# Kernel tuning notes

Measured on AMD Instinct MI355X. Metric: run time of the kernel, lower is better.

The kernel has to match this reference:

```python
import jax, jax.numpy as jnp
import numpy as np

TEMPERATURE = 8.0  # sqrt(head_dim=64)

def setup_inputs() -> dict:
    key = jax.random.key(0)
    kq, kk, kv, km = jax.random.split(key, 4)
    B, H, S, D = 2, 16, 2048, 64
    q = jax.random.normal(kq, (B, H, S, D), dtype=jnp.float32)
    k = jax.random.normal(kk, (B, H, S, D), dtype=jnp.float32)
    v = jax.random.normal(kv, (B, H, S, D), dtype=jnp.float32)
    mask = jax.random.randint(km, (B, 1, 1, S), 0, 2, dtype=jnp.int32)
    return {"q": q, "k": k, "v": v, "mask": mask}

def reference(q, k, v, mask):
    # attn = softmax((q/T) @ k^T) with mask fill of -1e9 (dropout p=0 -> no-op)
    attn = jnp.einsum("bhsd,bhtd->bhst", q / TEMPERATURE, k)  # [B,H,S,S]
    attn = jnp.where(mask == 0, jnp.float32(-1e9), attn)
    attn = jax.nn.softmax(attn, axis=-1)
    # output = v^T @ attn @ v  -> [B,H,D,D]
    out = jnp.einsum("bhsd,bhst->bhdt", v, attn)   # v.transpose(2,3) @ attn
    out = jnp.einsum("bhdt,bhtc->bhdc", out, v)     # @ v
    return (out, attn)
```

## Files before the change

kernel.cpp:

```cpp
#include <hip/hip_runtime.h>
#include <math.h>

#define S_LEN 2048
#define D_DIM 64
#define NBH   32
#define TINV  0.125f

typedef float  f32x4   __attribute__((ext_vector_type(4)));
typedef float  f32x16  __attribute__((ext_vector_type(16)));
typedef short  s16x4   __attribute__((ext_vector_type(4)));
typedef short  s16x8   __attribute__((ext_vector_type(8)));
typedef unsigned u32x4 __attribute__((ext_vector_type(4)));
typedef __bf16 bf16x8  __attribute__((ext_vector_type(8)));

__device__ __forceinline__ short bfc(float f) {
  return __builtin_bit_cast(short, (__bf16)f);
}
__device__ __forceinline__ unsigned pk2(float lo, float hi) {
  return (unsigned)(unsigned short)bfc(lo) | ((unsigned)(unsigned short)bfc(hi) << 16);
}

__device__ __forceinline__ f32x4 mfma16(s16x8 a, s16x8 b, f32x4 c) {
  return __builtin_amdgcn_mfma_f32_16x16x32_bf16(
      __builtin_bit_cast(bf16x8, a), __builtin_bit_cast(bf16x8, b), c, 0, 0, 0);
}
__device__ __forceinline__ f32x16 mfma32(s16x8 a, s16x8 b, f32x16 c) {
  return __builtin_amdgcn_mfma_f32_32x32x16_bf16(
      __builtin_bit_cast(bf16x8, a), __builtin_bit_cast(bf16x8, b), c, 0, 0, 0);
}

__device__ __forceinline__ short* ldsp(short* base, int row, int byteoff) {
  return (short*)((char*)base + row * 128 + (byteoff ^ ((row & 7) << 4)));
}

__global__ __launch_bounds__(256) void prep(
    const float* __restrict__ k, const float* __restrict__ v,
    short* __restrict__ kb16, short* __restrict__ vT)
{
  const int bid = blockIdx.x;
  const int t   = bid & 1023;
  const int bh  = t >> 5;
  const int kt  = t & 31;
  const int tid = threadIdx.x;

  if (bid < 1024) {
    const int st  = tid >> 2;
    const int sd0 = (tid & 3) * 16;
    const float* kp = k + ((size_t)bh * S_LEN + kt * 64 + st) * D_DIM + sd0;
    s16x8 o0, o1;
    #pragma unroll
    for (int j = 0; j < 8; ++j) { o0[j] = bfc(kp[j]); o1[j] = bfc(kp[8 + j]); }
    short* dst = kb16 + ((size_t)bh * S_LEN + kt * 64 + st) * D_DIM + sd0;
    *(s16x8*)dst       = o0;
    *(s16x8*)(dst + 8) = o1;
  } else {
    const int vt0 = (tid & 15) * 4;
    const int vd0 = (tid >> 4) * 4;
    const float* vb = v + ((size_t)bh * S_LEN + kt * 64) * D_DIM;
    f32x4 vr[4];
    #pragma unroll
    for (int i = 0; i < 4; ++i)
      vr[i] = *(const f32x4*)(vb + (size_t)(vt0 + i) * D_DIM + vd0);
    #pragma unroll
    for (int j = 0; j < 4; ++j) {
      s16x4 pk;
      pk[0] = bfc(vr[0][j]); pk[1] = bfc(vr[1][j]);
      pk[2] = bfc(vr[2][j]); pk[3] = bfc(vr[3][j]);
      *(s16x4*)(vT + (size_t)(bh * 64 + vd0 + j) * S_LEN + kt * 64 + vt0) = pk;
    }
  }
}

__global__ __launch_bounds__(256, 4) void attn_fwd(
    const float* __restrict__ q, const short* __restrict__ kb16,
    const short* __restrict__ vT, const int* __restrict__ mask,
    float* __restrict__ attn_out, short* __restrict__ OT)
{
  __shared__ short KV[2][64][64];
  __shared__ float rspart[4][32];

  short* KlB = &KV[0][0][0];
  short* VlB = &KV[1][0][0];

  const int bid   = blockIdx.x;
  const int xcd   = bid & 7;
  const int chunk = bid >> 3;
  const int bh    = xcd * 4 + (chunk >> 5);
  const int qt    = chunk & 31;
  const int b     = bh >> 4;

  const int tid  = threadIdx.x;
  const int wave = tid >> 6;
  const int lane = tid & 63;
  const int lr   = lane & 15;
  const int lg   = lane >> 4;
  const int L31  = lane & 31;
  const int hi   = lane >> 5;
  const int Q0   = qt * 64;

  const int qtile = wave & 1;
  const int tt    = wave >> 1;

  const short* kbb  = kb16 + (size_t)bh * S_LEN * D_DIM;
  const short* vtb  = vT   + (size_t)bh * 64 * S_LEN;
  const int*   mrow = mask + b * S_LEN;

  s16x8 aqv[4];
  {
    const float* qp = q + ((size_t)bh * S_LEN + Q0 + qtile * 32 + L31) * D_DIM + hi * 8;
    #pragma unroll
    for (int ks = 0; ks < 4; ++ks) {
      f32x4 x0 = *(const f32x4*)(qp + ks * 16);
      f32x4 x1 = *(const f32x4*)(qp + ks * 16 + 4);
      s16x8 f;
      #pragma unroll
      for (int j = 0; j < 4; ++j) { f[j] = bfc(x0[j]); f[4 + j] = bfc(x1[j]); }
      aqv[ks] = f;
    }
  }

  f32x16 oacc[2];
  #pragma unroll
  for (int dt = 0; dt < 2; ++dt)
    #pragma unroll
    for (int r = 0; r < 16; ++r) oacc[dt][r] = 0.f;
  float rs = 0.f;

  const int st = tid >> 2;
  const int c0 = (tid & 3) * 32;

  s16x8 kr0, kr1, vr0, vr1;
  kr0 = *(const s16x8*)(kbb + (size_t)st * D_DIM + c0 / 2);
  kr1 = *(const s16x8*)(kbb + (size_t)st * D_DIM + c0 / 2 + 8);
  vr0 = *(const s16x8*)(vtb + (size_t)st * S_LEN + c0 / 2);
  vr1 = *(const s16x8*)(vtb + (size_t)st * S_LEN + c0 / 2 + 8);

  for (int kt = 0; kt < 32; ++kt) {
    __syncthreads();
    *(s16x8*)ldsp(KlB, st, c0)      = kr0;
    *(s16x8*)ldsp(KlB, st, c0 + 16) = kr1;
    *(s16x8*)ldsp(VlB, st, c0)      = vr0;
    *(s16x8*)ldsp(VlB, st, c0 + 16) = vr1;
    __syncthreads();

    if (kt + 1 < 32) {
      kr0 = *(const s16x8*)(kbb + (size_t)((kt + 1) * 64 + st) * D_DIM + c0 / 2);
      kr1 = *(const s16x8*)(kbb + (size_t)((kt + 1) * 64 + st) * D_DIM + c0 / 2 + 8);
      vr0 = *(const s16x8*)(vtb + (size_t)st * S_LEN + (kt + 1) * 64 + c0 / 2);
      vr1 = *(const s16x8*)(vtb + (size_t)st * S_LEN + (kt + 1) * 64 + c0 / 2 + 8);
    }
    const unsigned long long mbits = __ballot(mrow[kt * 64 + lane] != 0);

    f32x16 sacc;
    #pragma unroll
    for (int r = 0; r < 16; ++r) sacc[r] = 0.f;
    #pragma unroll
    for (int ks = 0; ks < 4; ++ks) {
      s16x8 ak = *(const s16x8*)ldsp(KlB, tt * 32 + L31, ks * 32 + hi * 16);
      sacc = mfma32(ak, aqv[ks], sacc);
    }

    const unsigned mloc = (unsigned)(mbits >> (tt * 32 + hi * 4));
    #pragma unroll
    for (int r = 0; r < 16; ++r) {
      float e = __expf(sacc[r] * TINV);
      e = ((mloc >> ((r & 3) + 8 * (r >> 2))) & 1u) ? e : 0.f;
      rs += e;
      sacc[r] = e;
    }

    unsigned a0 = pk2(sacc[0], sacc[1]),   b0 = pk2(sacc[4], sacc[5]);
    unsigned a1 = pk2(sacc[2], sacc[3]),   b1 = pk2(sacc[6], sacc[7]);
    unsigned a2 = pk2(sacc[8], sacc[9]),   b2 = pk2(sacc[12], sacc[13]);
    unsigned a3 = pk2(sacc[10], sacc[11]), b3 = pk2(sacc[14], sacc[15]);
    asm volatile("v_permlane32_swap_b32 %0, %1" : "+v"(a0), "+v"(b0));
    asm volatile("v_permlane32_swap_b32 %0, %1" : "+v"(a1), "+v"(b1));
    asm volatile("v_permlane32_swap_b32 %0, %1" : "+v"(a2), "+v"(b2));
    asm volatile("v_permlane32_swap_b32 %0, %1" : "+v"(a3), "+v"(b3));
    const s16x8 pb0 = __builtin_bit_cast(s16x8, (u32x4){a0, a1, b0, b1});
    const s16x8 pb1 = __builtin_bit_cast(s16x8, (u32x4){a2, a3, b2, b3});

    #pragma unroll
    for (int dt = 0; dt < 2; ++dt) {
      s16x8 bv0 = *(const s16x8*)ldsp(VlB, dt * 32 + L31, tt * 64 + hi * 16);
      s16x8 bv1 = *(const s16x8*)ldsp(VlB, dt * 32 + L31, tt * 64 + 32 + hi * 16);
      oacc[dt] = mfma32(bv0, pb0, oacc[dt]);
      oacc[dt] = mfma32(bv1, pb1, oacc[dt]);
    }
  }

  rs += __shfl_xor(rs, 32, 64);

  __syncthreads();
  if (lane < 32) rspart[wave][lane] = rs;
  float* oex = (float*)&KV[0][0][0];
  if (wave >= 2) {
    #pragma unroll
    for (int dt = 0; dt < 2; ++dt)
      #pragma unroll
      for (int r = 0; r < 16; ++r)
        oex[(wave - 2) * 2048 + dt * 1024 + r * 64 + lane] = oacc[dt][r];
  }
  __syncthreads();

  if (wave < 2) {
    const float rinvq = 1.0f / (rspart[wave][L31] + rspart[wave + 2][L31]);
    #pragma unroll
    for (int dt = 0; dt < 2; ++dt)
      #pragma unroll
      for (int r = 0; r < 16; ++r) {
        const int d = dt * 32 + (r & 3) + 8 * (r >> 2) + 4 * hi;
        float val = (oacc[dt][r] + oex[wave * 2048 + dt * 1024 + r * 64 + lane]) * rinvq;
        OT[(size_t)(bh * 64 + d) * S_LEN + Q0 + wave * 32 + L31] = bfc(val);
      }
  }

  const int qin = (wave & 1) * 16 + lr;
  const float rinv = 1.0f / (rspart[wave >> 1][qin] + rspart[(wave >> 1) + 2][qin]);

  s16x8 aq[2];
  {
    const float* qp = q + ((size_t)bh * S_LEN + Q0 + wave * 16 + lr) * D_DIM + lg * 8;
    #pragma unroll
    for (int kk = 0; kk < 2; ++kk) {
      f32x4 x0 = *(const f32x4*)(qp + kk * 32);
      f32x4 x1 = *(const f32x4*)(qp + kk * 32 + 4);
      s16x8 f;
      #pragma unroll
      for (int j = 0; j < 4; ++j) { f[j] = bfc(x0[j]); f[4 + j] = bfc(x1[j]); }
      aq[kk] = f;
    }
  }

  float* ap_out = attn_out + (size_t)bh * S_LEN * S_LEN +
                  (size_t)(Q0 + wave * 16 + lr) * S_LEN;

  for (int kt = 0; kt < 32; ++kt) {
    const unsigned long long mbits = __ballot(mrow[kt * 64 + lane] != 0);

    #pragma unroll
    for (int n = 0; n < 4; ++n) {
      f32x4 sacc = (f32x4){0.f, 0.f, 0.f, 0.f};
      #pragma unroll
      for (int kk = 0; kk < 2; ++kk) {
        s16x8 bk = *(const s16x8*)(kbb + (size_t)(kt * 64 + n * 16 + lr) * D_DIM +
                                   kk * 32 + lg * 8);
        sacc = mfma16(bk, aq[kk], sacc);
      }
      const unsigned nib = (unsigned)(mbits >> (n * 16 + lg * 4)) & 0xFu;
      f32x4 pv;
      #pragma unroll
      for (int reg = 0; reg < 4; ++reg) {
        float e = __expf(sacc[reg] * TINV);
        pv[reg] = (nib & (1u << reg)) ? e * rinv : 0.f;
      }
      __builtin_nontemporal_store(pv, (f32x4*)(ap_out + kt * 64 + n * 16 + lg * 4));
    }
  }
}

__global__ __launch_bounds__(256) void vo_gemm(
    const short* __restrict__ vT, const short* __restrict__ OT,
    float* __restrict__ out)
{
  const int bh   = blockIdx.x;
  const int tid  = threadIdx.x;
  const int wave = tid >> 6;
  const int lane = tid & 63;
  const int lr   = lane & 15;
  const int lg   = lane >> 4;

  const short* vb = vT + (size_t)(bh * 64) * S_LEN;
  const short* ob = OT + (size_t)(bh * 64) * S_LEN;

  f32x4 acc[4];
  #pragma unroll
  for (int n = 0; n < 4; ++n) acc[n] = (f32x4){0.f, 0.f, 0.f, 0.f};

  for (int s = 0; s < S_LEN; s += 32) {
    s16x8 a = *(const s16x8*)&vb[(size_t)(wave * 16 + lr) * S_LEN + s + lg * 8];
    #pragma unroll
    for (int n = 0; n < 4; ++n) {
      s16x8 bo = *(const s16x8*)&ob[(size_t)(n * 16 + lr) * S_LEN + s + lg * 8];
      acc[n] = mfma16(a, bo, acc[n]);
    }
  }

  #pragma unroll
  for (int n = 0; n < 4; ++n) {
    #pragma unroll
    for (int reg = 0; reg < 4; ++reg) {
      const int d = wave * 16 + lg * 4 + reg;
      const int c = n * 16 + lr;
      out[(size_t)(bh * 64 + d) * 64 + c] = acc[n][reg];
    }
  }
}

extern "C" void kernel_launch(void* const* d_in, const int* in_sizes, int n_in,
                              void* d_out, int out_size, void* d_ws, size_t ws_size,
                              hipStream_t stream) {
  (void)in_sizes; (void)n_in; (void)out_size; (void)ws_size;
  const float* q    = (const float*)d_in[0];
  const float* k    = (const float*)d_in[1];
  const float* v    = (const float*)d_in[2];
  const int*   mask = (const int*)d_in[3];

  float* out  = (float*)d_out;
  float* attn = out + (size_t)NBH * 64 * 64;

  short* OT   = (short*)d_ws;
  short* vT   = (short*)d_ws + (size_t)NBH * 64 * S_LEN;
  short* kb16 = (short*)d_ws + (size_t)NBH * 64 * S_LEN * 2;

  prep<<<dim3(2048), dim3(256), 0, stream>>>(k, v, kb16, vT);
  attn_fwd<<<dim3(1024), dim3(256), 0, stream>>>(q, kb16, vT, mask, attn, OT);
  vo_gemm<<<dim3(NBH), dim3(256), 0, stream>>>(vT, OT, out);
}
```

Before: 241.3 us.

## Split attention-probability write into separate high-occupancy kernel fused with V-O GEMM

Moves the normalized attention-matrix recomputation and store out of the O-accumulation kernel into a new kernel with 32-row tiles and higher occupancy, passing per-row log2 normalizers through workspace. The final V^T·O GEMM is folded into the same launch as extra blocks, removing one launch and overlapping that small GEMM with the store-bound pass. The exponent uses exp2 with a folded scale and log-sum offset instead of exp followed by a multiply. The trade-off is recomputing QK^T in a separate pass and a dependency on the tail blocks reading OT written by the previous kernel.

```diff
diff --git a/kernel.cpp b/kernel.cpp
--- a/kernel.cpp
+++ b/kernel.cpp
@@ -5,6 +5,7 @@
 #define D_DIM 64
 #define NBH   32
 #define TINV  0.125f
+#define C2    0.18033688011112042f
 
 typedef float  f32x4   __attribute__((ext_vector_type(4)));
 typedef float  f32x16  __attribute__((ext_vector_type(16)));
@@ -71,10 +72,10 @@
   }
 }
 
-__global__ __launch_bounds__(256, 4) void attn_fwd(
+__global__ __launch_bounds__(256, 4) void attn_o(
     const float* __restrict__ q, const short* __restrict__ kb16,
     const short* __restrict__ vT, const int* __restrict__ mask,
-    float* __restrict__ attn_out, short* __restrict__ OT)
+    short* __restrict__ OT, float* __restrict__ l2rs)
 {
   __shared__ short KV[2][64][64];
   __shared__ float rspart[4][32];
@@ -92,8 +93,6 @@
   const int tid  = threadIdx.x;
   const int wave = tid >> 6;
   const int lane = tid & 63;
-  const int lr   = lane & 15;
-  const int lg   = lane >> 4;
   const int L31  = lane & 31;
   const int hi   = lane >> 5;
   const int Q0   = qt * 64;
@@ -204,7 +203,10 @@
   __syncthreads();
 
   if (wave < 2) {
-    const float rinvq = 1.0f / (rspart[wave][L31] + rspart[wave + 2][L31]);
+    const float rsum = rspart[wave][L31] + rspart[wave + 2][L31];
+    const float rinvq = 1.0f / rsum;
+    if (hi == 0)
+      l2rs[(size_t)bh * S_LEN + Q0 + wave * 32 + L31] = -__log2f(rsum);
     #pragma unroll
     for (int dt = 0; dt < 2; ++dt)
       #pragma unroll
@@ -214,85 +216,99 @@
         OT[(size_t)(bh * 64 + d) * S_LEN + Q0 + wave * 32 + L31] = bfc(val);
       }
   }
-
-  const int qin = (wave & 1) * 16 + lr;
-  const float rinv = 1.0f / (rspart[wave >> 1][qin] + rspart[(wave >> 1) + 2][qin]);
-
-  s16x8 aq[2];
-  {
-    const float* qp = q + ((size_t)bh * S_LEN + Q0 + wave * 16 + lr) * D_DIM + lg * 8;
-    #pragma unroll
-    for (int kk = 0; kk < 2; ++kk) {
-      f32x4 x0 = *(const f32x4*)(qp + kk * 32);
-      f32x4 x1 = *(const f32x4*)(qp + kk * 32 + 4);
-      s16x8 f;
-      #pragma unroll
-      for (int j = 0; j < 4; ++j) { f[j] = bfc(x0[j]); f[4 + j] = bfc(x1[j]); }
-      aq[kk] = f;
-    }
-  }
-
-  float* ap_out = attn_out + (size_t)bh * S_LEN * S_LEN +
-                  (size_t)(Q0 + wave * 16 + lr) * S_LEN;
-
-  for (int kt = 0; kt < 32; ++kt) {
-    const unsigned long long mbits = __ballot(mrow[kt * 64 + lane] != 0);
-
-    #pragma unroll
-    for (int n = 0; n < 4; ++n) {
-      f32x4 sacc = (f32x4){0.f, 0.f, 0.f, 0.f};
-      #pragma unroll
-      for (int kk = 0; kk < 2; ++kk) {
-        s16x8 bk = *(const s16x8*)(kbb + (size_t)(kt * 64 + n * 16 + lr) * D_DIM +
-                                   kk * 32 + lg * 8);
-        sacc = mfma16(bk, aq[kk], sacc);
-      }
-      const unsigned nib = (unsigned)(mbits >> (n * 16 + lg * 4)) & 0xFu;
-      f32x4 pv;
-      #pragma unroll
-      for (int reg = 0; reg < 4; ++reg) {
-        float e = __expf(sacc[reg] * TINV);
-        pv[reg] = (nib & (1u << reg)) ? e * rinv : 0.f;
-      }
-      __builtin_nontemporal_store(pv, (f32x4*)(ap_out + kt * 64 + n * 16 + lg * 4));
-    }
-  }
-}
-
-__global__ __launch_bounds__(256) void vo_gemm(
+}
+
+__global__ __launch_bounds__(256, 8) void attn_p(
+    const float* __restrict__ q, const short* __restrict__ kb16,
+    const int* __restrict__ mask, const float* __restrict__ l2rs,
+    float* __restrict__ attn_out,
     const short* __restrict__ vT, const short* __restrict__ OT,
     float* __restrict__ out)
 {
-  const int bh   = blockIdx.x;
+  const int bid  = blockIdx.x;
   const int tid  = threadIdx.x;
   const int wave = tid >> 6;
   const int lane = tid & 63;
   const int lr   = lane & 15;
   const int lg   = lane >> 4;
 
-  const short* vb = vT + (size_t)(bh * 64) * S_LEN;
-  const short* ob = OT + (size_t)(bh * 64) * S_LEN;
-
-  f32x4 acc[4];
-  #pragma unroll
-  for (int n = 0; n < 4; ++n) acc[n] = (f32x4){0.f, 0.f, 0.f, 0.f};
-
-  for (int s = 0; s < S_LEN; s += 32) {
-    s16x8 a = *(const s16x8*)&vb[(size_t)(wave * 16 + lr) * S_LEN + s + lg * 8];
-    #pragma unroll
-    for (int n = 0; n < 4; ++n) {
-      s16x8 bo = *(const s16x8*)&ob[(size_t)(n * 16 + lr) * S_LEN + s + lg * 8];
-      acc[n] = mfma16(a, bo, acc[n]);
-    }
-  }
-
-  #pragma unroll
-  for (int n = 0; n < 4; ++n) {
-    #pragma unroll
-    for (int reg = 0; reg < 4; ++reg) {
-      const int d = wave * 16 + lg * 4 + reg;
-      const int c = n * 16 + lr;
-      out[(size_t)(bh * 64 + d) * 64 + c] = acc[n][reg];
+  if (bid >= 2048) {
+    const int bh = bid - 2048;
+    const short* vb = vT + (size_t)(bh * 64) * S_LEN;
+    const short* ob = OT + (size_t)(bh * 64) * S_LEN;
+    f32x4 acc[4];
+    #pragma unroll
+    for (int n = 0; n < 4; ++n) acc[n] = (f32x4){0.f, 0.f, 0.f, 0.f};
+    for (int s = 0; s < S_LEN; s += 32) {
+      s16x8 a = *(const s16x8*)&vb[(size_t)(wave * 16 + lr) * S_LEN + s + lg * 8];
+      #pragma unroll
+      for (int n = 0; n < 4; ++n) {
+        s16x8 bo = *(const s16x8*)&ob[(size_t)(n * 16 + lr) * S_LEN + s + lg * 8];
+        acc[n] = mfma16(a, bo, acc[n]);
+      }
+    }
+    #pragma unroll
+    for (int n = 0; n < 4; ++n)
+      #pragma unroll
+      for (int reg = 0; reg < 4; ++reg) {
+        const int d = wave * 16 + lg * 4 + reg;
+        const int c = n * 16 + lr;
+        out[(size_t)(bh * 64 + d) * 64 + c] = acc[n][reg];
+      }
+    return;
+  }
+
+  const int xcd   = bid & 7;
+  const int chunk = bid >> 3;
+  const int bh    = xcd * 4 + (chunk >> 6);
+  const int qb    = chunk & 63;
+  const int b     = bh >> 4;
+  const int qh    = wave & 1;
+  const int th    = wave >> 1;
+  const int Q0    = qb * 32;
+  const int qrow  = Q0 + qh * 16 + lr;
+
+  const short* kbb  = kb16 + (size_t)bh * S_LEN * D_DIM;
+  const int*   mrow = mask + b * S_LEN;
+
+  s16x8 aq[2];
+  {
+    const float* qp = q + ((size_t)bh * S_LEN + qrow) * D_DIM + lg * 8;
+    #pragma unroll
+    for (int kk = 0; kk < 2; ++kk) {
+      f32x4 x0 = *(const f32x4*)(qp + kk * 32);
+      f32x4 x1 = *(const f32x4*)(qp + kk * 32 + 4);
+      s16x8 f;
+      #pragma unroll
+      for (int j = 0; j < 4; ++j) { f[j] = bfc(x0[j]); f[4 + j] = bfc(x1[j]); }
+      aq[kk] = f;
+    }
+  }
+
+  const float l2r = l2rs[(size_t)bh * S_LEN + qrow];
+  float* ap_out = attn_out + (size_t)bh * S_LEN * S_LEN + (size_t)qrow * S_LEN;
+
+  for (int kt = 0; kt < 32; ++kt) {
+    const unsigned long long mbits = __ballot(mrow[kt * 64 + lane] != 0);
+
+    #pragma unroll
+    for (int n = 0; n < 2; ++n) {
+      const int trow = th * 32 + n * 16;
+      f32x4 sacc = (f32x4){0.f, 0.f, 0.f, 0.f};
+      #pragma unroll
+      for (int kk = 0; kk < 2; ++kk) {
+        s16x8 bk = *(const s16x8*)(kbb + (size_t)(kt * 64 + trow + lr) * D_DIM +
+                                   kk * 32 + lg * 8);
+        sacc = mfma16(bk, aq[kk], sacc);
+      }
+      const unsigned nib = (unsigned)(mbits >> (trow + lg * 4)) & 0xFu;
+      f32x4 pv;
+      #pragma unroll
+      for (int reg = 0; reg < 4; ++reg) {
+        float e = __builtin_amdgcn_exp2f(fmaf(sacc[reg], C2, l2r));
+        pv[reg] = (nib & (1u << reg)) ? e : 0.f;
+      }
+      __builtin_nontemporal_store(pv, (f32x4*)(ap_out + kt * 64 + trow + lg * 4));
     }
   }
 }
@@ -309,11 +325,13 @@
   float* out  = (float*)d_out;
   float* attn = out + (size_t)NBH * 64 * 64;
 
+  const size_t HS = (size_t)NBH * 64 * S_LEN;
   short* OT   = (short*)d_ws;
-  short* vT   = (short*)d_ws + (size_t)NBH * 64 * S_LEN;
-  short* kb16 = (short*)d_ws + (size_t)NBH * 64 * S_LEN * 2;
+  short* vT   = OT + HS;
+  short* kb16 = vT + HS;
+  float* l2rs = (float*)(kb16 + HS);
 
   prep<<<dim3(2048), dim3(256), 0, stream>>>(k, v, kb16, vT);
-  attn_fwd<<<dim3(1024), dim3(256), 0, stream>>>(q, kb16, vT, mask, attn, OT);
-  vo_gemm<<<dim3(NBH), dim3(256), 0, stream>>>(vT, OT, out);
-}
+  attn_o<<<dim3(1024), dim3(256), 0, stream>>>(q, kb16, vT, mask, OT, l2rs);
+  attn_p<<<dim3(2080), dim3(256), 0, stream>>>(q, kb16, mask, l2rs, attn, vT, OT, out);
+}
```

New measurement: 305.2 us. +26.5%, slower.

## Stage attention tile through swizzled LDS for coalesced row stores; fold normalizer into exp2

Applied to the files above, without the earlier changes.

The attention-probability write-out is restaged: each wave writes its 16x64 tile into a per-wave XOR-swizzled LDS buffer, then reads it back so that each store instruction covers contiguous 256-byte row segments instead of scattered 16-byte pieces. The exp and reciprocal multiply are replaced by a single exp2 of (s*log2e/T - log2(rowsum)), which removes the per-element multiply. This adds an LDS round trip per key tile and an extra block barrier, and relies on reusing the KV shared buffer after the barrier.

```diff
diff --git a/kernel.cpp b/kernel.cpp
--- a/kernel.cpp
+++ b/kernel.cpp
@@ -5,6 +5,7 @@
 #define D_DIM 64
 #define NBH   32
 #define TINV  0.125f
+#define C2    0.18033688011112042f
 
 typedef float  f32x4   __attribute__((ext_vector_type(4)));
 typedef float  f32x16  __attribute__((ext_vector_type(16)));
@@ -204,7 +205,8 @@
   __syncthreads();
 
   if (wave < 2) {
-    const float rinvq = 1.0f / (rspart[wave][L31] + rspart[wave + 2][L31]);
+    const float rsum = rspart[wave][L31] + rspart[wave + 2][L31];
+    const float rinvq = 1.0f / rsum;
     #pragma unroll
     for (int dt = 0; dt < 2; ++dt)
       #pragma unroll
@@ -216,7 +218,9 @@
   }
 
   const int qin = (wave & 1) * 16 + lr;
-  const float rinv = 1.0f / (rspart[wave >> 1][qin] + rspart[(wave >> 1) + 2][qin]);
+  const float l2r = -__log2f(rspart[wave >> 1][qin] + rspart[(wave >> 1) + 2][qin]);
+
+  __syncthreads();
 
   s16x8 aq[2];
   {
@@ -232,8 +236,10 @@
     }
   }
 
-  float* ap_out = attn_out + (size_t)bh * S_LEN * S_LEN +
-                  (size_t)(Q0 + wave * 16 + lr) * S_LEN;
+  char* stb = (char*)&KV[0][0][0] + wave * 4096;
+  float* abase = attn_out + (size_t)bh * S_LEN * S_LEN + (size_t)(Q0 + wave * 16) * S_LEN;
+  const int rrow = lane >> 4;
+  const int rcol = lane & 15;
 
   for (int kt = 0; kt < 32; ++kt) {
     const unsigned long long mbits = __ballot(mrow[kt * 64 + lane] != 0);
@@ -251,10 +257,18 @@
       f32x4 pv;
       #pragma unroll
       for (int reg = 0; reg < 4; ++reg) {
-        float e = __expf(sacc[reg] * TINV);
-        pv[reg] = (nib & (1u << reg)) ? e * rinv : 0.f;
+        float e = __builtin_amdgcn_exp2f(fmaf(sacc[reg], C2, l2r));
+        pv[reg] = (nib & (1u << reg)) ? e : 0.f;
       }
-      __builtin_nontemporal_store(pv, (f32x4*)(ap_out + kt * 64 + n * 16 + lg * 4));
+      *(f32x4*)(stb + lr * 256 + ((n * 64 + lg * 16) ^ ((lr & 7) << 4))) = pv;
+    }
+
+    #pragma unroll
+    for (int i = 0; i < 4; ++i) {
+      const int row = i * 4 + rrow;
+      f32x4 val = *(const f32x4*)(stb + row * 256 + ((rcol * 16) ^ ((row & 7) << 4)));
+      __builtin_nontemporal_store(val,
+          (f32x4*)(abase + (size_t)row * S_LEN + kt * 64 + rcol * 4));
     }
   }
 }
@@ -309,9 +323,10 @@
   float* out  = (float*)d_out;
   float* attn = out + (size_t)NBH * 64 * 64;
 
+  const size_t HS = (size_t)NBH * 64 * S_LEN;
   short* OT   = (short*)d_ws;
-  short* vT   = (short*)d_ws + (size_t)NBH * 64 * S_LEN;
-  short* kb16 = (short*)d_ws + (size_t)NBH * 64 * S_LEN * 2;
+  short* vT   = OT + HS;
+  short* kb16 = vT + HS;
 
   prep<<<dim3(2048), dim3(256), 0, stream>>>(k, v, kb16, vT);
   attn_fwd<<<dim3(1024), dim3(256), 0, stream>>>(q, kb16, vT, mask, attn, OT);
```

After: 223.9 us. -7.2%, faster.
